# Performance work log

Measured on AMD Instinct MI355X. Metric: run time of the kernel, lower is better.

The kernel has to match this reference:

```python
import jax, jax.numpy as jnp
import numpy as np

L, N, D_IN, D_H = 512, 64, 512, 512


def setup_inputs() -> dict:
    key = jax.random.key(0)
    ks = jax.random.split(key, 12)
    s_in = 1.0 / np.sqrt(D_IN + D_H)
    s_out = 1.0 / np.sqrt(D_H)
    inp = {
        "x": jax.random.normal(ks[0], (L, N, D_IN), dtype=jnp.float32),
        "h0": jnp.zeros((N, D_H), dtype=jnp.float32),
        "c0": jnp.zeros((N, D_H), dtype=jnp.float32),
        "W_f": jax.random.uniform(ks[1], (D_IN + D_H, D_H), jnp.float32, -s_in, s_in),
        "b_f": jax.random.uniform(ks[2], (D_H,), jnp.float32, -s_in, s_in),
        "W_c": jax.random.uniform(ks[3], (D_IN + D_H, D_H), jnp.float32, -s_in, s_in),
        "b_c": jax.random.uniform(ks[4], (D_H,), jnp.float32, -s_in, s_in),
        "W_i": jax.random.uniform(ks[5], (D_IN + D_H, D_H), jnp.float32, -s_in, s_in),
        "b_i": jax.random.uniform(ks[6], (D_H,), jnp.float32, -s_in, s_in),
        "W_o": jax.random.uniform(ks[7], (D_IN + D_H, D_H), jnp.float32, -s_in, s_in),
        "b_o": jax.random.uniform(ks[8], (D_H,), jnp.float32, -s_in, s_in),
        "W_out": jax.random.uniform(ks[9], (D_H, D_IN), jnp.float32, -s_out, s_out),
        "b_out": jax.random.uniform(ks[10], (D_IN,), jnp.float32, -s_out, s_out),
    }
    return inp


def reference(x, h0, c0, W_f, b_f, W_c, b_c, W_i, b_i, W_o, b_o, W_out, b_out):
    # Fuse the 4 gate linears into one GEMM per step: [f, c~, i, o] order.
    W_gates = jnp.concatenate([W_f, W_c, W_i, W_o], axis=1)  # (D_IN+D_H, 4*D_H)
    b_gates = jnp.concatenate([b_f, b_c, b_i, b_o], axis=0)  # (4*D_H,)
    d_h = h0.shape[-1]

    def step(carry, x_t):
        h, c = carry
        z = jnp.concatenate([x_t, h], axis=1) @ W_gates + b_gates  # (N, 4*D_H)
        f_t = jax.nn.sigmoid(z[:, 0 * d_h:1 * d_h])
        C_t = jnp.tanh(z[:, 1 * d_h:2 * d_h])
        i_t = jax.nn.sigmoid(z[:, 2 * d_h:3 * d_h])
        o_t = jax.nn.sigmoid(z[:, 3 * d_h:4 * d_h])
        c = f_t * c + i_t * C_t
        h = o_t * jnp.tanh(c)
        return (h, c), h

    (h, c), hs = jax.lax.scan(step, (h0, c0), x)  # hs: (L, N, D_H)
    outputs = hs @ W_out + b_out  # (L, N, D_IN)
    return outputs, h, c
```

## Files before the change

### kernel.cpp

```cpp
#include <hip/hip_runtime.h>

typedef float  f32x4  __attribute__((ext_vector_type(4)));
typedef short  bf16x8 __attribute__((ext_vector_type(8)));

#define DEVI static __device__ __forceinline__

namespace {
constexpr int kL   = 512;
constexpr int kN   = 64;
constexpr int kDH  = 512;
constexpr int kDIN = 512;
constexpr int kG   = 2048;
constexpr int kT   = 32;
constexpr int kChunks = kL / kT;
constexpr int kHS  = kN * kDH;
constexpr int kFP = 16;
constexpr size_t kOutSz = (size_t)kL * kN * kDIN;
}


DEVI unsigned short f2bf(float f) {
  union { float f; unsigned u; } v; v.f = f;
  unsigned r = v.u + 0x7FFFu + ((v.u >> 16) & 1u);
  return (unsigned short)(r >> 16);
}
DEVI float sigm(float z) { return 1.f / (1.f + __expf(-z)); }
DEVI float tanh_f(float z) { return 2.f / (1.f + __expf(-2.f * z)) - 1.f; }

__global__ void prep_kernel(
    const float* __restrict__ Wf, const float* __restrict__ Wc,
    const float* __restrict__ Wi, const float* __restrict__ Wo,
    const float* __restrict__ bf, const float* __restrict__ bc,
    const float* __restrict__ bi, const float* __restrict__ bo,
    const float* __restrict__ Wout,
    const float* __restrict__ h0, const float* __restrict__ c0,
    unsigned short* __restrict__ WxT, unsigned short* __restrict__ WoT,
    unsigned short* __restrict__ WhB, float* __restrict__ bg,
    unsigned short* __restrict__ hsx, float* __restrict__ cbuf,
    unsigned int* __restrict__ flags)
{
  const int gid = blockIdx.x * blockDim.x + threadIdx.x;
  const int stride = gridDim.x * blockDim.x;
  const float* Wg[4]  = {Wf, Wc, Wi, Wo};
  const float* bgs[4] = {bf, bc, bi, bo};

  for (int i = gid; i < 64 * kFP; i += stride) flags[i] = 0u;

  for (int i = gid; i < kG * 512; i += stride) {
    int k = i >> 11, g = i & 2047;
    WxT[(size_t)g * 512 + k] = f2bf(Wg[g >> 9][(size_t)k * 512 + (g & 511)]);
  }
  for (int i = gid; i < 512 * 512; i += stride) {
    int k = i >> 9, c = i & 511;
    WoT[(size_t)c * 512 + k] = f2bf(Wout[(size_t)k * 512 + c]);
  }
  for (int i = gid; i < 4 * 512 * 512; i += stride) {
    int hcol = i & 511;
    int gate = (i >> 9) & 3;
    int k    = i >> 11;
    int cg = hcol >> 3, jj = hcol & 7;
    int n  = gate * 8 + jj;
    int kblk = k >> 3, kin = k & 7;
    size_t dst = ((size_t)cg * 32 + n) * 512 + (((kblk ^ (n & 7)) << 3) | kin);
    WhB[dst] = f2bf(Wg[gate][(size_t)(512 + k) * 512 + hcol]);
  }
  for (int i = gid; i < kG; i += stride) bg[i] = bgs[i >> 9][i & 511];
  for (int i = gid; i < kN * kDH; i += stride) {
    int n = i >> 9, c = i & 511;
    hsx[((size_t)(c >> 3)) * 512 + ((n >> 4) * 128) + ((n & 15) * 8) + (c & 7)]
        = f2bf(h0[i]);
    cbuf[i] = c0[i];
  }
}

struct SMem {
  union {
    unsigned short WT[32 * 512];
    struct { unsigned short Ash[128][40]; unsigned short Bsh[128][40]; } g;
  };
};

DEVI void gemm_x_tile(SMem& sm, const float* __restrict__ X,
                      const unsigned short* __restrict__ WxT,
                      const float* __restrict__ bg,
                      float* __restrict__ Zx2, int row0, int col0, int tid)
{
  const int lane = tid & 63, wave = tid >> 6;
  const int wr = wave >> 1, wc = wave & 1;
  const int m16 = lane & 15, kg = (lane >> 4) * 8;

  f32x4 acc[4][4] = {};

  for (int k0 = 0; k0 < 512; k0 += 32) {
    __syncthreads();
    #pragma unroll
    for (int i = 0; i < 4; ++i) {
      int idx = i * 256 + tid;
      int r = idx >> 3, kq = idx & 7;
      float4 v = *(const float4*)&X[(size_t)(row0 + r) * 512 + k0 + kq * 4];
      unsigned short* dst = &sm.g.Ash[r][kq * 4];
      dst[0] = f2bf(v.x); dst[1] = f2bf(v.y); dst[2] = f2bf(v.z); dst[3] = f2bf(v.w);
    }
    #pragma unroll
    for (int i = 0; i < 2; ++i) {
      int idx = i * 256 + tid;
      int c = idx >> 2, kq = idx & 3;
      *(uint4*)&sm.g.Bsh[c][kq * 8] =
          *(const uint4*)&WxT[(size_t)(col0 + c) * 512 + k0 + kq * 8];
    }
    __syncthreads();
    bf16x8 fa[4], fb[4];
    #pragma unroll
    for (int mi = 0; mi < 4; ++mi) fa[mi] = *(const bf16x8*)&sm.g.Ash[wr*64 + mi*16 + m16][kg];
    #pragma unroll
    for (int ni = 0; ni < 4; ++ni) fb[ni] = *(const bf16x8*)&sm.g.Bsh[wc*64 + ni*16 + m16][kg];
    #pragma unroll
    for (int mi = 0; mi < 4; ++mi)
      #pragma unroll
      for (int ni = 0; ni < 4; ++ni)
        acc[mi][ni] = __builtin_amdgcn_mfma_f32_16x16x32_bf16(fa[mi], fb[ni], acc[mi][ni], 0, 0, 0);
  }
  const int rg = (lane >> 4) * 4;
  #pragma unroll
  for (int ni = 0; ni < 4; ++ni) {
    int col = col0 + wc*64 + ni*16 + m16;
    float bb = bg[col];
    int gate = col >> 9, hcol = col & 511;
    int cg = hcol >> 3, n = gate * 8 + (hcol & 7);
    int qn = n & 15, half = n >> 4;
    #pragma unroll
    for (int mi = 0; mi < 4; ++mi)
      #pragma unroll
      for (int r = 0; r < 4; ++r) {
        int row = row0 + wr*64 + mi*16 + rg + r;
        int t = row >> 6, b = row & 63;
        int wv = b >> 4, lgv = (b >> 2) & 3, iv = b & 3;
        Zx2[((size_t)(cg * 32 + t) * 256 + (wv * 64 + lgv * 16 + qn)) * 8 +
            iv * 2 + half] = acc[mi][ni][r] + bb;
      }
  }
}

__global__ __launch_bounds__(256) void gemm_x_kernel(
    const float* __restrict__ X, const unsigned short* __restrict__ WxT,
    const float* __restrict__ bg, float* __restrict__ Zx2)
{
  __shared__ SMem sm;
  gemm_x_tile(sm, X, WxT, bg, Zx2, blockIdx.x * 128, blockIdx.y * 128, threadIdx.x);
}

__global__ __launch_bounds__(256, 1) void lstm_fused_kernel(
    const unsigned short* __restrict__ WhB,
    const float* __restrict__ Zxcur,
    unsigned short* __restrict__ hsx,
    float* __restrict__ cbuf,
    int step0,
    unsigned int* __restrict__ flags,
    float* __restrict__ dout,
    const float* __restrict__ Xnext,
    const unsigned short* __restrict__ WxT,
    const float* __restrict__ bg,
    float* __restrict__ Zxnext)
{
  __shared__ SMem sm;
  const int tid = threadIdx.x;

  if (blockIdx.x >= 64) {
    if (Xnext == nullptr) return;
    for (int tile = (int)blockIdx.x - 64; tile < 256; tile += 192) {
      gemm_x_tile(sm, Xnext, WxT, bg, Zxnext, (tile >> 4) * 128, (tile & 15) * 128, tid);
      __syncthreads();
    }
    return;
  }

  const int cg = blockIdx.x;
  const int j0 = cg * 8;
  const int w   = tid >> 6;
  const int l   = tid & 63;
  const int q   = l & 15;
  const int lg  = l >> 4;
  const int jj  = q & 7;
  const int i0  = (q < 8) ? 0 : 2;

  {
    const uint4* wsrc = (const uint4*)(WhB + (size_t)cg * 32 * 512);
    uint4* wdst = (uint4*)sm.WT;
    #pragma unroll
    for (int i = 0; i < 8; ++i) wdst[i * 256 + tid] = wsrc[i * 256 + tid];
  }
  const size_t cidx = (size_t)(w * 16 + lg * 4 + i0) * 512 + j0 + jj;
  float c0r = cbuf[cidx];
  float c1r = cbuf[cidx + 512];
  __syncthreads();

  bf16x8 B0[16], B1[16];
  #pragma unroll
  for (int s = 0; s < 16; ++s) {
    const int kb = 4 * s + lg;
    B0[s] = *(const bf16x8*)&sm.WT[(size_t)q * 512 + ((kb ^ jj) << 3)];
    B1[s] = *(const bf16x8*)&sm.WT[(size_t)(16 + q) * 512 + ((kb ^ jj) << 3)];
  }

  const float* zbase = Zxcur + (size_t)cg * 32 * 2048 + (size_t)tid * 8;

  float zc0[4], zc1[4];
  {
    f32x4 a = *(const f32x4*)zbase;
    f32x4 b = *(const f32x4*)(zbase + 4);
    zc0[0] = a[0]; zc1[0] = a[1]; zc0[1] = a[2]; zc1[1] = a[3];
    zc0[2] = b[0]; zc1[2] = b[1]; zc0[3] = b[2]; zc1[3] = b[3];
  }

  for (int t = 0; t < kT; ++t) {
    const int st = step0 + t;

    if (t > 0) {
      if (tid < 64) {
        for (;;) {
          int fv = (int)__hip_atomic_load(&flags[l * kFP], __ATOMIC_RELAXED,
                                          __HIP_MEMORY_SCOPE_AGENT);
          if (__all(fv >= st)) break;
        }
      }
      __syncthreads();
    }

    const unsigned short* hrow =
        hsx + (size_t)st * kHS + (size_t)lg * 512 + w * 128 + q * 8;
    bf16x8 A[16];
    #pragma unroll
    for (int s = 0; s < 16; ++s) A[s] = *(const bf16x8*)(hrow + 2048 * s);

    float zn0[4], zn1[4];
    if (t + 1 < kT) {
      const float* zb = zbase + (size_t)(t + 1) * 2048;
      f32x4 a = *(const f32x4*)zb;
      f32x4 b = *(const f32x4*)(zb + 4);
      zn0[0] = a[0]; zn1[0] = a[1]; zn0[1] = a[2]; zn1[1] = a[3];
      zn0[2] = b[0]; zn1[2] = b[1]; zn0[3] = b[2]; zn1[3] = b[3];
    }

    f32x4 acc0 = {}, acc1 = {};
    #pragma unroll
    for (int s = 0; s < 16; ++s) {
      acc0 = __builtin_amdgcn_mfma_f32_16x16x32_bf16(A[s], B0[s], acc0, 0, 0, 0);
      acc1 = __builtin_amdgcn_mfma_f32_16x16x32_bf16(A[s], B1[s], acc1, 0, 0, 0);
    }

    float t0[4], t1[4], ot0[4], ot1[4];
    #pragma unroll
    for (int i = 0; i < 4; ++i) { t0[i] = acc0[i] + zc0[i]; t1[i] = acc1[i] + zc1[i]; }
    #pragma unroll
    for (int i = 0; i < 4; ++i) {
      ot0[i] = __shfl_xor(t0[i], 8, 64);
      ot1[i] = __shfl_xor(t1[i], 8, 64);
    }
    float hh[2];
    #pragma unroll
    for (int u = 0; u < 2; ++u) {
      const int i = i0 + u;
      float zf = (q < 8) ? t0[i] : ot0[i];
      float zc = (q < 8) ? ot0[i] : t0[i];
      float zi = (q < 8) ? t1[i] : ot1[i];
      float zo = (q < 8) ? ot1[i] : t1[i];
      float fg = sigm(zf), ig = sigm(zi), og = sigm(zo);
      float Ct = tanh_f(zc);
      float& cr = u ? c1r : c0r;
      cr = fg * cr + ig * Ct;
      hh[u] = og * tanh_f(cr);
    }

    {
      unsigned short hb0 = f2bf(hh[0]), hb1 = f2bf(hh[1]);
      unsigned o0 = (unsigned)(unsigned short)__shfl_xor((int)hb0, 1, 64);
      unsigned o1 = (unsigned)(unsigned short)__shfl_xor((int)hb1, 1, 64);
      if ((q & 1) == 0) {
        const size_t base = (size_t)(st + 1) * kHS + (size_t)cg * 512 +
                            w * 128 + (lg * 4 + i0) * 8 + jj;
        __hip_atomic_store((unsigned*)&hsx[base], ((unsigned)hb0) | (o0 << 16),
                           __ATOMIC_RELAXED, __HIP_MEMORY_SCOPE_AGENT);
        __hip_atomic_store((unsigned*)&hsx[base + 8], ((unsigned)hb1) | (o1 << 16),
                           __ATOMIC_RELAXED, __HIP_MEMORY_SCOPE_AGENT);
      }
      if (st == kL - 1) {
        dout[kOutSz + cidx] = hh[0];
        dout[kOutSz + cidx + 512] = hh[1];
        dout[kOutSz + (size_t)kN * kDH + cidx] = c0r;
        dout[kOutSz + (size_t)kN * kDH + cidx + 512] = c1r;
      }
    }

    asm volatile("s_waitcnt vmcnt(0)" ::: "memory");
    __syncthreads();
    if (tid == 0)
      __hip_atomic_store(&flags[cg * kFP], (unsigned)(st + 1), __ATOMIC_RELAXED,
                         __HIP_MEMORY_SCOPE_AGENT);

    if (t + 1 < kT) {
      #pragma unroll
      for (int i = 0; i < 4; ++i) { zc0[i] = zn0[i]; zc1[i] = zn1[i]; }
    }
  }

  cbuf[cidx] = c0r;
  cbuf[cidx + 512] = c1r;
}

__global__ __launch_bounds__(256) void gemm_out_kernel(
    const unsigned short* __restrict__ Hs,
    const unsigned short* __restrict__ WoT,
    const float* __restrict__ bout,
    float* __restrict__ out)
{
  __shared__ unsigned short Ash[128][40];
  __shared__ unsigned short Bsh[128][40];
  const int row0 = blockIdx.x * 128, col0 = blockIdx.y * 128;
  const int tid = threadIdx.x;
  const int lane = tid & 63, wave = tid >> 6;
  const int wr = wave >> 1, wc = wave & 1;
  const int m16 = lane & 15, kg = (lane >> 4) * 8;

  f32x4 acc[4][4] = {};

  for (int k0 = 0; k0 < 512; k0 += 32) {
    __syncthreads();
    #pragma unroll
    for (int i = 0; i < 2; ++i) {
      int idx = i * 256 + tid;
      int r = idx >> 2, kq = idx & 3;
      int grow = row0 + r;
      size_t src = (size_t)(grow >> 6) * kHS + (size_t)((k0 >> 3) + kq) * 512 +
                   ((grow >> 4) & 3) * 128 + (grow & 15) * 8;
      *(uint4*)&Ash[r][kq * 8] = *(const uint4*)&Hs[src];
    }
    #pragma unroll
    for (int i = 0; i < 2; ++i) {
      int idx = i * 256 + tid;
      int c = idx >> 2, kq = idx & 3;
      *(uint4*)&Bsh[c][kq * 8] =
          *(const uint4*)&WoT[(size_t)(col0 + c) * 512 + k0 + kq * 8];
    }
    __syncthreads();
    bf16x8 fa[4], fb[4];
    #pragma unroll
    for (int mi = 0; mi < 4; ++mi) fa[mi] = *(const bf16x8*)&Ash[wr*64 + mi*16 + m16][kg];
    #pragma unroll
    for (int ni = 0; ni < 4; ++ni) fb[ni] = *(const bf16x8*)&Bsh[wc*64 + ni*16 + m16][kg];
    #pragma unroll
    for (int mi = 0; mi < 4; ++mi)
      #pragma unroll
      for (int ni = 0; ni < 4; ++ni)
        acc[mi][ni] = __builtin_amdgcn_mfma_f32_16x16x32_bf16(fa[mi], fb[ni], acc[mi][ni], 0, 0, 0);
  }
  const int rg = (lane >> 4) * 4;
  #pragma unroll
  for (int ni = 0; ni < 4; ++ni) {
    int col = col0 + wc*64 + ni*16 + m16;
    float bb = bout[col];
    #pragma unroll
    for (int mi = 0; mi < 4; ++mi)
      #pragma unroll
      for (int r = 0; r < 4; ++r)
        out[(size_t)(row0 + wr*64 + mi*16 + rg + r) * 512 + col] = acc[mi][ni][r] + bb;
  }
}

extern "C" void kernel_launch(void* const* d_in, const int* in_sizes, int n_in,
                              void* d_out, int out_size, void* d_ws, size_t ws_size,
                              hipStream_t stream) {
  (void)in_sizes; (void)n_in; (void)out_size; (void)ws_size;
  const float* x    = (const float*)d_in[0];
  const float* h0   = (const float*)d_in[1];
  const float* c0   = (const float*)d_in[2];
  const float* Wf   = (const float*)d_in[3];
  const float* bf_  = (const float*)d_in[4];
  const float* Wc   = (const float*)d_in[5];
  const float* bc_  = (const float*)d_in[6];
  const float* Wi_  = (const float*)d_in[7];
  const float* bi_  = (const float*)d_in[8];
  const float* Wo   = (const float*)d_in[9];
  const float* bo_  = (const float*)d_in[10];
  const float* Wout = (const float*)d_in[11];
  const float* bout = (const float*)d_in[12];
  float* out = (float*)d_out;

  char* ws = (char*)d_ws;
  size_t off = 0;
  auto alloc = [&](size_t bytes) -> void* {
    void* p = ws + off;
    off += (bytes + 255) & ~(size_t)255;
    return p;
  };
  float*          ZxA = (float*)alloc((size_t)kT * kN * kG * 4);
  float*          ZxB = (float*)alloc((size_t)kT * kN * kG * 4);
  unsigned short* hsx = (unsigned short*)alloc((size_t)(kL + 1) * kN * kDH * 2);
  unsigned short* WxT = (unsigned short*)alloc((size_t)kG * 512 * 2);
  unsigned short* WoT = (unsigned short*)alloc((size_t)512 * 512 * 2);
  unsigned short* WhB = (unsigned short*)alloc((size_t)64 * 32 * 512 * 2);
  float*          bg  = (float*)alloc((size_t)kG * 4);
  float*          cbf = (float*)alloc((size_t)kN * kDH * 4);
  unsigned int*   flg = (unsigned int*)alloc((size_t)64 * kFP * 4);

  prep_kernel<<<1024, 256, 0, stream>>>(Wf, Wc, Wi_, Wo, bf_, bc_, bi_, bo_,
                                        Wout, h0, c0, WxT, WoT, WhB, bg, hsx, cbf, flg);
  gemm_x_kernel<<<dim3(16, 16), 256, 0, stream>>>(x, WxT, bg, ZxA);
  for (int c = 0; c < kChunks; ++c) {
    float* Zxcur = (c & 1) ? ZxB : ZxA;
    float* Zxnxt = (c & 1) ? ZxA : ZxB;
    const float* xnext = (c + 1 < kChunks)
        ? x + (size_t)(c + 1) * kT * kN * kDIN : nullptr;
    lstm_fused_kernel<<<256, 256, 0, stream>>>(
        WhB, Zxcur, hsx, cbf, c * kT, flg, out, xnext, WxT, bg, Zxnxt);
  }
  gemm_out_kernel<<<dim3(256, 4), 256, 0, stream>>>(
      hsx + (size_t)kN * kDH, WoT, bout, out);
}
```

Baseline: 1.727 ms.

## Merge per-chunk LSTM launches into one persistent kernel with flag-based Zx handoff

After: 1.752 ms. Within noise of the previous version (+1.5%).

```diff
diff --git a/kernel.cpp b/kernel.cpp
--- a/kernel.cpp
+++ b/kernel.cpp
@@ -37,7 +37,7 @@
     unsigned short* __restrict__ WxT, unsigned short* __restrict__ WoT,
     unsigned short* __restrict__ WhB, float* __restrict__ bg,
     unsigned short* __restrict__ hsx, float* __restrict__ cbuf,
-    unsigned int* __restrict__ flags)
+    unsigned int* __restrict__ flags, unsigned int* __restrict__ zxcnt)
 {
   const int gid = blockIdx.x * blockDim.x + threadIdx.x;
   const int stride = gridDim.x * blockDim.x;
@@ -45,6 +45,7 @@
   const float* bgs[4] = {bf, bc, bi, bo};
 
   for (int i = gid; i < 64 * kFP; i += stride) flags[i] = 0u;
+  for (int i = gid; i < kChunks * kFP; i += stride) zxcnt[i] = 0u;
 
   for (int i = gid; i < kG * 512; i += stride) {
     int k = i >> 11, g = i & 2047;
@@ -141,35 +142,51 @@
   }
 }
 
-__global__ __launch_bounds__(256) void gemm_x_kernel(
-    const float* __restrict__ X, const unsigned short* __restrict__ WxT,
-    const float* __restrict__ bg, float* __restrict__ Zx2)
-{
-  __shared__ SMem sm;
-  gemm_x_tile(sm, X, WxT, bg, Zx2, blockIdx.x * 128, blockIdx.y * 128, threadIdx.x);
-}
-
-__global__ __launch_bounds__(256, 1) void lstm_fused_kernel(
+__global__ __launch_bounds__(256, 1) void lstm_persist_kernel(
     const unsigned short* __restrict__ WhB,
-    const float* __restrict__ Zxcur,
+    float* __restrict__ ZxA,
+    float* __restrict__ ZxB,
     unsigned short* __restrict__ hsx,
-    float* __restrict__ cbuf,
-    int step0,
+    const float* __restrict__ cbuf,
     unsigned int* __restrict__ flags,
+    unsigned int* __restrict__ zxcnt,
     float* __restrict__ dout,
-    const float* __restrict__ Xnext,
+    const float* __restrict__ x,
     const unsigned short* __restrict__ WxT,
-    const float* __restrict__ bg,
-    float* __restrict__ Zxnext)
+    const float* __restrict__ bg)
 {
   __shared__ SMem sm;
   const int tid = threadIdx.x;
+  const int l   = tid & 63;
 
   if (blockIdx.x >= 64) {
-    if (Xnext == nullptr) return;
-    for (int tile = (int)blockIdx.x - 64; tile < 256; tile += 192) {
-      gemm_x_tile(sm, Xnext, WxT, bg, Zxnext, (tile >> 4) * 128, (tile & 15) * 128, tid);
+    const int btile = (int)blockIdx.x - 64;
+    for (int cn = 0; cn < kChunks; ++cn) {
+      float* Zbuf = (cn & 1) ? ZxB : ZxA;
+      const float* Xc = x + (size_t)cn * kT * kN * kDIN;
+      if (cn >= 2) {
+        const int need = (cn - 1) * kT;
+        if (tid < 64) {
+          for (;;) {
+            int fv = (int)__hip_atomic_load(&flags[l * kFP], __ATOMIC_RELAXED,
+                                            __HIP_MEMORY_SCOPE_AGENT);
+            if (__all(fv >= need)) break;
+            __builtin_amdgcn_s_sleep(64);
+          }
+        }
+        __syncthreads();
+      }
+      int ntiles = 0;
+      for (int tile = btile; tile < 256; tile += 192) {
+        gemm_x_tile(sm, Xc, WxT, bg, Zbuf, (tile >> 4) * 128, (tile & 15) * 128, tid);
+        __syncthreads();
+        ++ntiles;
+      }
+      asm volatile("s_waitcnt vmcnt(0)" ::: "memory");
       __syncthreads();
+      if (tid == 0)
+        __hip_atomic_fetch_add(&zxcnt[cn * kFP], (unsigned)ntiles,
+                               __ATOMIC_RELAXED, __HIP_MEMORY_SCOPE_AGENT);
     }
     return;
   }
@@ -177,7 +194,6 @@
   const int cg = blockIdx.x;
   const int j0 = cg * 8;
   const int w   = tid >> 6;
-  const int l   = tid & 63;
   const int q   = l & 15;
   const int lg  = l >> 4;
   const int jj  = q & 7;
@@ -202,8 +218,15 @@
     B1[s] = *(const bf16x8*)&sm.WT[(size_t)(16 + q) * 512 + ((kb ^ jj) << 3)];
   }
 
-  const float* zbase = Zxcur + (size_t)cg * 32 * 2048 + (size_t)tid * 8;
-
+  {
+    for (;;) {
+      unsigned v = __hip_atomic_load(&zxcnt[0], __ATOMIC_RELAXED,
+                                     __HIP_MEMORY_SCOPE_AGENT);
+      if (v >= 256u) break;
+      __builtin_amdgcn_s_sleep(32);
+    }
+  }
+  const float* zbase = ZxA + (size_t)cg * 32 * 2048 + (size_t)tid * 8;
   float zc0[4], zc1[4];
   {
     f32x4 a = *(const f32x4*)zbase;
@@ -212,15 +235,19 @@
     zc0[2] = b[0]; zc1[2] = b[1]; zc0[3] = b[2]; zc1[3] = b[3];
   }
 
-  for (int t = 0; t < kT; ++t) {
-    const int st = step0 + t;
-
-    if (t > 0) {
+  for (int st = 0; st < kL; ++st) {
+    const int tloc  = st & (kT - 1);
+    const int chunk = st >> 5;
+
+    if (st > 0) {
       if (tid < 64) {
+        int fv = (int)__hip_atomic_load(&flags[l * kFP], __ATOMIC_RELAXED,
+                                        __HIP_MEMORY_SCOPE_AGENT);
         for (;;) {
-          int fv = (int)__hip_atomic_load(&flags[l * kFP], __ATOMIC_RELAXED,
+          int fn = (int)__hip_atomic_load(&flags[l * kFP], __ATOMIC_RELAXED,
                                           __HIP_MEMORY_SCOPE_AGENT);
           if (__all(fv >= st)) break;
+          fv = fn;
         }
       }
       __syncthreads();
@@ -233,8 +260,22 @@
     for (int s = 0; s < 16; ++s) A[s] = *(const bf16x8*)(hrow + 2048 * s);
 
     float zn0[4], zn1[4];
-    if (t + 1 < kT) {
-      const float* zb = zbase + (size_t)(t + 1) * 2048;
+    const float* zbase_next = zbase;
+    if (st + 1 < kL) {
+      const float* zb;
+      if (tloc == kT - 1) {
+        zbase_next = (((chunk + 1) & 1) ? ZxB : ZxA) +
+                     (size_t)cg * 32 * 2048 + (size_t)tid * 8;
+        for (;;) {
+          unsigned v = __hip_atomic_load(&zxcnt[(chunk + 1) * kFP],
+                                         __ATOMIC_RELAXED,
+                                         __HIP_MEMORY_SCOPE_AGENT);
+          if (v >= 256u) break;
+        }
+        zb = zbase_next;
+      } else {
+        zb = zbase + (size_t)(tloc + 1) * 2048;
+      }
       f32x4 a = *(const f32x4*)zb;
       f32x4 b = *(const f32x4*)(zb + 4);
       zn0[0] = a[0]; zn1[0] = a[1]; zn0[1] = a[2]; zn1[1] = a[3];
@@ -297,14 +338,12 @@
       __hip_atomic_store(&flags[cg * kFP], (unsigned)(st + 1), __ATOMIC_RELAXED,
                          __HIP_MEMORY_SCOPE_AGENT);
 
-    if (t + 1 < kT) {
+    if (st + 1 < kL) {
       #pragma unroll
       for (int i = 0; i < 4; ++i) { zc0[i] = zn0[i]; zc1[i] = zn1[i]; }
-    }
-  }
-
-  cbuf[cidx] = c0r;
-  cbuf[cidx + 512] = c1r;
+      zbase = zbase_next;
+    }
+  }
 }
 
 __global__ __launch_bounds__(256) void gemm_out_kernel(
@@ -401,18 +440,13 @@
   float*          bg  = (float*)alloc((size_t)kG * 4);
   float*          cbf = (float*)alloc((size_t)kN * kDH * 4);
   unsigned int*   flg = (unsigned int*)alloc((size_t)64 * kFP * 4);
+  unsigned int*   zxc = (unsigned int*)alloc((size_t)kChunks * kFP * 4);
 
   prep_kernel<<<1024, 256, 0, stream>>>(Wf, Wc, Wi_, Wo, bf_, bc_, bi_, bo_,
-                                        Wout, h0, c0, WxT, WoT, WhB, bg, hsx, cbf, flg);
-  gemm_x_kernel<<<dim3(16, 16), 256, 0, stream>>>(x, WxT, bg, ZxA);
-  for (int c = 0; c < kChunks; ++c) {
-    float* Zxcur = (c & 1) ? ZxB : ZxA;
-    float* Zxnxt = (c & 1) ? ZxA : ZxB;
-    const float* xnext = (c + 1 < kChunks)
-        ? x + (size_t)(c + 1) * kT * kN * kDIN : nullptr;
-    lstm_fused_kernel<<<256, 256, 0, stream>>>(
-        WhB, Zxcur, hsx, cbf, c * kT, flg, out, xnext, WxT, bg, Zxnxt);
-  }
+                                        Wout, h0, c0, WxT, WoT, WhB, bg, hsx,
+                                        cbf, flg, zxc);
+  lstm_persist_kernel<<<256, 256, 0, stream>>>(
+      WhB, ZxA, ZxB, hsx, cbf, flg, zxc, out, x, WxT, bg);
   gemm_out_kernel<<<dim3(256, 4), 256, 0, stream>>>(
       hsx + (size_t)kN * kDH, WoT, bout, out);
 }
```

## Pack two column groups per recurrent block to halve flag synchronisation

Applied to the files above, without the earlier changes.

New measurement: 2.288 ms. +32.5%, slower.

```diff
diff --git a/kernel.cpp b/kernel.cpp
--- a/kernel.cpp
+++ b/kernel.cpp
@@ -14,7 +14,8 @@
 constexpr int kT   = 32;
 constexpr int kChunks = kL / kT;
 constexpr int kHS  = kN * kDH;
-constexpr int kFP = 16;
+constexpr int kFP  = 16;
+constexpr int kRB  = 32;
 constexpr size_t kOutSz = (size_t)kL * kN * kDIN;
 }
 
@@ -44,7 +45,7 @@
   const float* Wg[4]  = {Wf, Wc, Wi, Wo};
   const float* bgs[4] = {bf, bc, bi, bo};
 
-  for (int i = gid; i < 64 * kFP; i += stride) flags[i] = 0u;
+  for (int i = gid; i < kRB * kFP; i += stride) flags[i] = 0u;
 
   for (int i = gid; i < kG * 512; i += stride) {
     int k = i >> 11, g = i & 2047;
@@ -73,17 +74,16 @@
   }
 }
 
-struct SMem {
-  union {
-    unsigned short WT[32 * 512];
-    struct { unsigned short Ash[128][40]; unsigned short Bsh[128][40]; } g;
-  };
+struct GS {
+  unsigned short Ash[128][40];
+  unsigned short Bsh[128][40];
 };
 
-DEVI void gemm_x_tile(SMem& sm, const float* __restrict__ X,
+DEVI void gemm_x_tile(GS& sm, const float* __restrict__ X,
                       const unsigned short* __restrict__ WxT,
                       const float* __restrict__ bg,
-                      float* __restrict__ Zx2, int row0, int col0, int tid)
+                      float* __restrict__ Zx2, int row0, int col0, int tid,
+                      bool active)
 {
   const int lane = tid & 63, wave = tid >> 6;
   const int wr = wave >> 1, wc = wave & 1;
@@ -93,33 +93,36 @@
 
   for (int k0 = 0; k0 < 512; k0 += 32) {
     __syncthreads();
-    #pragma unroll
-    for (int i = 0; i < 4; ++i) {
-      int idx = i * 256 + tid;
-      int r = idx >> 3, kq = idx & 7;
-      float4 v = *(const float4*)&X[(size_t)(row0 + r) * 512 + k0 + kq * 4];
-      unsigned short* dst = &sm.g.Ash[r][kq * 4];
-      dst[0] = f2bf(v.x); dst[1] = f2bf(v.y); dst[2] = f2bf(v.z); dst[3] = f2bf(v.w);
-    }
-    #pragma unroll
-    for (int i = 0; i < 2; ++i) {
-      int idx = i * 256 + tid;
-      int c = idx >> 2, kq = idx & 3;
-      *(uint4*)&sm.g.Bsh[c][kq * 8] =
-          *(const uint4*)&WxT[(size_t)(col0 + c) * 512 + k0 + kq * 8];
+    if (active) {
+      #pragma unroll
+      for (int i = 0; i < 4; ++i) {
+        int idx = i * 256 + tid;
+        int r = idx >> 3, kq = idx & 7;
+        float4 v = *(const float4*)&X[(size_t)(row0 + r) * 512 + k0 + kq * 4];
+        unsigned short* dst = &sm.Ash[r][kq * 4];
+        dst[0] = f2bf(v.x); dst[1] = f2bf(v.y); dst[2] = f2bf(v.z); dst[3] = f2bf(v.w);
+      }
+      #pragma unroll
+      for (int i = 0; i < 2; ++i) {
+        int idx = i * 256 + tid;
+        int c = idx >> 2, kq = idx & 3;
+        *(uint4*)&sm.Bsh[c][kq * 8] =
+            *(const uint4*)&WxT[(size_t)(col0 + c) * 512 + k0 + kq * 8];
+      }
     }
     __syncthreads();
     bf16x8 fa[4], fb[4];
     #pragma unroll
-    for (int mi = 0; mi < 4; ++mi) fa[mi] = *(const bf16x8*)&sm.g.Ash[wr*64 + mi*16 + m16][kg];
-    #pragma unroll
-    for (int ni = 0; ni < 4; ++ni) fb[ni] = *(const bf16x8*)&sm.g.Bsh[wc*64 + ni*16 + m16][kg];
+    for (int mi = 0; mi < 4; ++mi) fa[mi] = *(const bf16x8*)&sm.Ash[wr*64 + mi*16 + m16][kg];
+    #pragma unroll
+    for (int ni = 0; ni < 4; ++ni) fb[ni] = *(const bf16x8*)&sm.Bsh[wc*64 + ni*16 + m16][kg];
     #pragma unroll
     for (int mi = 0; mi < 4; ++mi)
       #pragma unroll
       for (int ni = 0; ni < 4; ++ni)
         acc[mi][ni] = __builtin_amdgcn_mfma_f32_16x16x32_bf16(fa[mi], fb[ni], acc[mi][ni], 0, 0, 0);
   }
+  if (!active) return;
   const int rg = (lane >> 4) * 4;
   #pragma unroll
   for (int ni = 0; ni < 4; ++ni) {
@@ -145,11 +148,12 @@
     const float* __restrict__ X, const unsigned short* __restrict__ WxT,
     const float* __restrict__ bg, float* __restrict__ Zx2)
 {
-  __shared__ SMem sm;
-  gemm_x_tile(sm, X, WxT, bg, Zx2, blockIdx.x * 128, blockIdx.y * 128, threadIdx.x);
-}
-
-__global__ __launch_bounds__(256, 1) void lstm_fused_kernel(
+  __shared__ GS sm;
+  gemm_x_tile(sm, X, WxT, bg, Zx2, blockIdx.x * 128, blockIdx.y * 128,
+              threadIdx.x, true);
+}
+
+__global__ __launch_bounds__(512, 1) void lstm_fused_kernel(
     const unsigned short* __restrict__ WhB,
     const float* __restrict__ Zxcur,
     unsigned short* __restrict__ hsx,
@@ -162,48 +166,49 @@
     const float* __restrict__ bg,
     float* __restrict__ Zxnext)
 {
-  __shared__ SMem sm;
+  __shared__ GS sm2[2];
   const int tid = threadIdx.x;
 
-  if (blockIdx.x >= 64) {
+  if (blockIdx.x >= kRB) {
     if (Xnext == nullptr) return;
-    for (int tile = (int)blockIdx.x - 64; tile < 256; tile += 192) {
-      gemm_x_tile(sm, Xnext, WxT, bg, Zxnext, (tile >> 4) * 128, (tile & 15) * 128, tid);
+    const int half = tid >> 8, t256 = tid & 255;
+    const int worker = ((int)blockIdx.x - kRB) * 2 + half;
+    #pragma unroll 1
+    for (int i = 0; i < 2; ++i) {
+      int tile = worker + i * 192;
+      bool active = (tile < 256);
+      gemm_x_tile(sm2[half], Xnext, WxT, bg, Zxnext,
+                  (tile >> 4) * 128, (tile & 15) * 128, t256, active);
       __syncthreads();
     }
     return;
   }
 
-  const int cg = blockIdx.x;
+  const int bi = blockIdx.x;
+  const int v  = tid >> 6;
+  const int l  = tid & 63;
+  const int w  = v & 3;
+  const int cg = bi * 2 + (v >> 2);
   const int j0 = cg * 8;
-  const int w   = tid >> 6;
-  const int l   = tid & 63;
-  const int q   = l & 15;
-  const int lg  = l >> 4;
-  const int jj  = q & 7;
-  const int i0  = (q < 8) ? 0 : 2;
-
-  {
-    const uint4* wsrc = (const uint4*)(WhB + (size_t)cg * 32 * 512);
-    uint4* wdst = (uint4*)sm.WT;
-    #pragma unroll
-    for (int i = 0; i < 8; ++i) wdst[i * 256 + tid] = wsrc[i * 256 + tid];
-  }
-  const size_t cidx = (size_t)(w * 16 + lg * 4 + i0) * 512 + j0 + jj;
-  float c0r = cbuf[cidx];
-  float c1r = cbuf[cidx + 512];
-  __syncthreads();
-
+  const int q  = l & 15;
+  const int lg = l >> 4;
+  const int jj = q & 7;
+  const int i0 = (q < 8) ? 0 : 2;
+
+  const unsigned short* Wgp = WhB + (size_t)cg * 32 * 512;
   bf16x8 B0[16], B1[16];
   #pragma unroll
   for (int s = 0; s < 16; ++s) {
     const int kb = 4 * s + lg;
-    B0[s] = *(const bf16x8*)&sm.WT[(size_t)q * 512 + ((kb ^ jj) << 3)];
-    B1[s] = *(const bf16x8*)&sm.WT[(size_t)(16 + q) * 512 + ((kb ^ jj) << 3)];
-  }
-
-  const float* zbase = Zxcur + (size_t)cg * 32 * 2048 + (size_t)tid * 8;
-
+    B0[s] = *(const bf16x8*)&Wgp[(size_t)q * 512 + ((kb ^ jj) << 3)];
+    B1[s] = *(const bf16x8*)&Wgp[(size_t)(16 + q) * 512 + ((kb ^ jj) << 3)];
+  }
+
+  const size_t cidx = (size_t)(w * 16 + lg * 4 + i0) * 512 + j0 + jj;
+  float c0r = cbuf[cidx];
+  float c1r = cbuf[cidx + 512];
+
+  const float* zbase = Zxcur + (size_t)cg * 32 * 2048 + (size_t)(w * 64 + l) * 8;
   float zc0[4], zc1[4];
   {
     f32x4 a = *(const f32x4*)zbase;
@@ -218,7 +223,8 @@
     if (t > 0) {
       if (tid < 64) {
         for (;;) {
-          int fv = (int)__hip_atomic_load(&flags[l * kFP], __ATOMIC_RELAXED,
+          int fv = (int)__hip_atomic_load(&flags[(l & 31) * kFP],
+                                          __ATOMIC_RELAXED,
                                           __HIP_MEMORY_SCOPE_AGENT);
           if (__all(fv >= st)) break;
         }
@@ -294,7 +300,7 @@
     asm volatile("s_waitcnt vmcnt(0)" ::: "memory");
     __syncthreads();
     if (tid == 0)
-      __hip_atomic_store(&flags[cg * kFP], (unsigned)(st + 1), __ATOMIC_RELAXED,
+      __hip_atomic_store(&flags[bi * kFP], (unsigned)(st + 1), __ATOMIC_RELAXED,
                          __HIP_MEMORY_SCOPE_AGENT);
 
     if (t + 1 < kT) {
@@ -400,7 +406,7 @@
   unsigned short* WhB = (unsigned short*)alloc((size_t)64 * 32 * 512 * 2);
   float*          bg  = (float*)alloc((size_t)kG * 4);
   float*          cbf = (float*)alloc((size_t)kN * kDH * 4);
-  unsigned int*   flg = (unsigned int*)alloc((size_t)64 * kFP * 4);
+  unsigned int*   flg = (unsigned int*)alloc((size_t)kRB * kFP * 4);
 
   prep_kernel<<<1024, 256, 0, stream>>>(Wf, Wc, Wi_, Wo, bf_, bc_, bi_, bo_,
                                         Wout, h0, c0, WxT, WoT, WhB, bg, hsx, cbf, flg);
@@ -410,7 +416,7 @@
     float* Zxnxt = (c & 1) ? ZxA : ZxB;
     const float* xnext = (c + 1 < kChunks)
         ? x + (size_t)(c + 1) * kT * kN * kDIN : nullptr;
-    lstm_fused_kernel<<<256, 256, 0, stream>>>(
+    lstm_fused_kernel<<<128, 512, 0, stream>>>(
         WhB, Zxcur, hsx, cbf, c * kT, flg, out, xnext, WxT, bg, Zxnxt);
   }
   gemm_out_kernel<<<dim3(256, 4), 256, 0, stream>>>(
```

## Replace per-step block barrier with per-group readiness tokens for staged h loads

Applied to the files above, without the earlier changes.

Measured after the change: 1.785 ms. +3.4%, slower.

```diff
diff --git a/kernel.cpp b/kernel.cpp
--- a/kernel.cpp
+++ b/kernel.cpp
@@ -163,6 +163,7 @@
     float* __restrict__ Zxnext)
 {
   __shared__ SMem sm;
+  __shared__ unsigned tok[4];
   const int tid = threadIdx.x;
 
   if (blockIdx.x >= 64) {
@@ -189,6 +190,7 @@
     #pragma unroll
     for (int i = 0; i < 8; ++i) wdst[i * 256 + tid] = wsrc[i * 256 + tid];
   }
+  if (tid < 4) tok[tid] = 0u;
   const size_t cidx = (size_t)(w * 16 + lg * 4 + i0) * 512 + j0 + jj;
   float c0r = cbuf[cidx];
   float c1r = cbuf[cidx + 512];
@@ -212,25 +214,79 @@
     zc0[2] = b[0]; zc1[2] = b[1]; zc0[3] = b[2]; zc1[3] = b[3];
   }
 
+#define LOADG(g)                                                      \
+  do {                                                                \
+    A[4*(g)+0] = *(const bf16x8*)(hrow + 2048 * (4*(g)+0));           \
+    A[4*(g)+1] = *(const bf16x8*)(hrow + 2048 * (4*(g)+1));           \
+    A[4*(g)+2] = *(const bf16x8*)(hrow + 2048 * (4*(g)+2));           \
+    A[4*(g)+3] = *(const bf16x8*)(hrow + 2048 * (4*(g)+3));           \
+  } while (0)
+
   for (int t = 0; t < kT; ++t) {
     const int st = step0 + t;
-
-    if (t > 0) {
-      if (tid < 64) {
-        for (;;) {
-          int fv = (int)__hip_atomic_load(&flags[l * kFP], __ATOMIC_RELAXED,
-                                          __HIP_MEMORY_SCOPE_AGENT);
-          if (__all(fv >= st)) break;
-        }
-      }
-      __syncthreads();
-    }
 
     const unsigned short* hrow =
         hsx + (size_t)st * kHS + (size_t)lg * 512 + w * 128 + q * 8;
     bf16x8 A[16];
-    #pragma unroll
-    for (int s = 0; s < 16; ++s) A[s] = *(const bf16x8*)(hrow + 2048 * s);
+
+    if (t > 0) {
+      if (w == 0) {
+        unsigned rdy = 0;
+        auto refresh = [&]() {
+          int fv = (int)__hip_atomic_load(&flags[l * kFP], __ATOMIC_RELAXED,
+                                          __HIP_MEMORY_SCOPE_AGENT);
+          unsigned long long bl = __ballot(fv >= st);
+          unsigned nr = 0;
+          if (((bl >>  0) & 0xFFFFull) == 0xFFFFull) nr |= 1u;
+          if (((bl >> 16) & 0xFFFFull) == 0xFFFFull) nr |= 2u;
+          if (((bl >> 32) & 0xFFFFull) == 0xFFFFull) nr |= 4u;
+          if (((bl >> 48) & 0xFFFFull) == 0xFFFFull) nr |= 8u;
+          unsigned nw = nr & ~rdy;
+          if (nw && l == 0) {
+            if (nw & 1u) __hip_atomic_store(&tok[0], (unsigned)st,
+                             __ATOMIC_RELAXED, __HIP_MEMORY_SCOPE_WORKGROUP);
+            if (nw & 2u) __hip_atomic_store(&tok[1], (unsigned)st,
+                             __ATOMIC_RELAXED, __HIP_MEMORY_SCOPE_WORKGROUP);
+            if (nw & 4u) __hip_atomic_store(&tok[2], (unsigned)st,
+                             __ATOMIC_RELAXED, __HIP_MEMORY_SCOPE_WORKGROUP);
+            if (nw & 8u) __hip_atomic_store(&tok[3], (unsigned)st,
+                             __ATOMIC_RELAXED, __HIP_MEMORY_SCOPE_WORKGROUP);
+          }
+          rdy |= nr;
+        };
+        while (!(rdy & 1u)) refresh();
+        asm volatile("" ::: "memory");
+        LOADG(0);
+        while (!(rdy & 2u)) refresh();
+        asm volatile("" ::: "memory");
+        LOADG(1);
+        while (!(rdy & 4u)) refresh();
+        asm volatile("" ::: "memory");
+        LOADG(2);
+        while (!(rdy & 8u)) refresh();
+        asm volatile("" ::: "memory");
+        LOADG(3);
+      } else {
+        while (__hip_atomic_load(&tok[0], __ATOMIC_RELAXED,
+                                 __HIP_MEMORY_SCOPE_WORKGROUP) < (unsigned)st) {}
+        asm volatile("" ::: "memory");
+        LOADG(0);
+        while (__hip_atomic_load(&tok[1], __ATOMIC_RELAXED,
+                                 __HIP_MEMORY_SCOPE_WORKGROUP) < (unsigned)st) {}
+        asm volatile("" ::: "memory");
+        LOADG(1);
+        while (__hip_atomic_load(&tok[2], __ATOMIC_RELAXED,
+                                 __HIP_MEMORY_SCOPE_WORKGROUP) < (unsigned)st) {}
+        asm volatile("" ::: "memory");
+        LOADG(2);
+        while (__hip_atomic_load(&tok[3], __ATOMIC_RELAXED,
+                                 __HIP_MEMORY_SCOPE_WORKGROUP) < (unsigned)st) {}
+        asm volatile("" ::: "memory");
+        LOADG(3);
+      }
+    } else {
+      LOADG(0); LOADG(1); LOADG(2); LOADG(3);
+    }
 
     float zn0[4], zn1[4];
     if (t + 1 < kT) {
@@ -302,6 +358,7 @@
       for (int i = 0; i < 4; ++i) { zc0[i] = zn0[i]; zc1[i] = zn1[i]; }
     }
   }
+#undef LOADG
 
   cbuf[cidx] = c0r;
   cbuf[cidx + 512] = c1r;
```
